# Kernel tuning notes

Hardware: AMD Instinct MI355X
Metric: run time of the kernel (lower is better)

Reference implementation:

```python
import jax, jax.numpy as jnp
import numpy as np

N, K, C = 100000, 16, 64
H, MID = 64, 16
EPS_BN = 1e-5
EPS_NORM = 1e-12

def _normalize(x, axis=-1):
    n = jnp.linalg.norm(x, axis=axis, keepdims=True)
    return x / jnp.maximum(n, EPS_NORM)

def _bn_nck(x, g, b):
    # BatchNorm1d on [N, C, K]: stats over (N, K) per channel, training mode
    m = jnp.mean(x, axis=(0, 2), keepdims=True)
    v = jnp.var(x, axis=(0, 2), keepdims=True)
    return (x - m) / jnp.sqrt(v + EPS_BN) * g[None, :, None] + b[None, :, None]

def _bn_nc(x, g, b):
    m = jnp.mean(x, axis=0, keepdims=True)
    v = jnp.var(x, axis=0, keepdims=True)
    return (x - m) / jnp.sqrt(v + EPS_BN) * g[None, :] + b[None, :]

def _conv_bn_relu(x, W, b, g, be):
    # 1x1 Conv1d: x [N, Cin, K], W [Cout, Cin]
    y = jnp.einsum('oc,nck->nok', W, x) + b[None, :, None]
    return jax.nn.relu(_bn_nck(y, g, be))

def setup_inputs():
    ks = jax.random.split(jax.random.key(0), 16)
    rn = lambda k, s: jax.random.normal(k, s, dtype=jnp.float32) * 0.05
    z = lambda n: jnp.zeros((n,), jnp.float32)
    o = lambda n: jnp.ones((n,), jnp.float32)
    return {
        'xyz': jax.random.normal(ks[0], (N, 3), jnp.float32),
        'cov': jax.random.normal(ks[1], (N, 3, 3), jnp.float32),
        'feats': jax.random.normal(ks[2], (N, C), jnp.float32),
        'knn_indices': jax.random.randint(ks[3], (N, K), 0, N),
        'fw1': rn(ks[4], (H, C)), 'fb1': z(H), 'fg1': o(H), 'fbe1': z(H),
        'fw2': rn(ks[5], (H, H)), 'fb2': z(H), 'fg2': o(H), 'fbe2': z(H),
        'ww1': rn(ks[6], (8, 14)), 'wb1': z(8), 'wg1': o(8), 'wbe1': z(8),
        'ww2': rn(ks[7], (8, 8)), 'wb2': z(8), 'wg2': o(8), 'wbe2': z(8),
        'ww3': rn(ks[8], (MID, 8)), 'wb3': z(MID), 'wg3': o(MID), 'wbe3': z(MID),
        'lin_w': rn(ks[9], (H, MID * H)), 'lin_b': z(H),
        'bng': o(H), 'bnb': z(H),
    }

def reference(xyz, cov, feats, knn_indices,
              fw1, fb1, fg1, fbe1, fw2, fb2, fg2, fbe2,
              ww1, wb1, wg1, wbe1, ww2, wb2, wg2, wbe2,
              ww3, wb3, wg3, wbe3, lin_w, lin_b, bng, bnb):
    xg = xyz[knn_indices]                      # [N,K,3] gathered positions
    loc = xg - xg[:, :1, :]                    # localized xyz (center = neighbor 0)
    cg = cov[knn_indices]                      # [N,K,3,3]
    fg = feats[knn_indices]                    # [N,K,C]

    n_alpha = fg[:, :, 3:6]                    # neighbor normals
    n_miu = n_alpha[:, 0, :]                   # center normal [N,3]
    r_hat = _normalize(loc, axis=2)
    dot_nm_rhat = jnp.einsum('nd,nkd->nk', n_miu, r_hat)
    v_miu = _normalize(n_miu[:, None, :] - dot_nm_rhat[:, :, None] * r_hat, axis=2)
    w_miu = _normalize(jnp.cross(r_hat, v_miu), axis=2)

    t1 = jnp.einsum('nkd,nd->nk', n_alpha, n_miu)
    t2 = dot_nm_rhat
    t3 = jnp.sum(r_hat * n_alpha, axis=2)
    t4 = jnp.einsum('nkd,nd->nk', loc, n_miu)
    t5 = t3
    t6 = jnp.sum(n_alpha * v_miu, axis=2)
    t7 = jnp.sum(n_alpha * w_miu, axis=2)
    t8 = jnp.sum(loc * jnp.cross(n_alpha, jnp.broadcast_to(n_miu[:, None, :], n_alpha.shape)), axis=2)
    t9 = jnp.linalg.norm(loc, axis=2)
    s1 = jnp.einsum('nkd,nkde,nke->nk', loc, cg, loc)        # per-neighbor cov quad form
    s2 = jnp.einsum('nkd,nde,nke->nk', loc, cg[:, 0], loc)   # center cov quad form

    win = jnp.concatenate([loc.transpose(0, 2, 1),
                           jnp.stack([t1, t2, t3, t4, t5, t6, t7, t8, t9, s1, s2], axis=1)],
                          axis=1)              # [N,14,K]

    w = _conv_bn_relu(win, ww1, wb1, wg1, wbe1)
    w = _conv_bn_relu(w, ww2, wb2, wg2, wbe2)
    w = _conv_bn_relu(w, ww3, wb3, wg3, wbe3)  # [N,MID,K]

    f = _conv_bn_relu(fg.transpose(0, 2, 1), fw1, fb1, fg1, fbe1)
    f = _conv_bn_relu(f, fw2, fb2, fg2, fbe2)  # [N,H,K]

    new = jnp.einsum('nhk,nmk->nhm', f, w).reshape(f.shape[0], -1)  # [N, H*MID]
    return jax.nn.relu(_bn_nc(new @ lin_w.T + lin_b, bng, bnb))
```

## Files before the change

### kernel.cpp

```cpp
#include <hip/hip_runtime.h>
#include <hip/hip_bf16.h>

typedef __hip_bfloat16 bf16;
typedef __attribute__((ext_vector_type(8))) short bf16x8;
typedef __attribute__((ext_vector_type(4))) short bf16x4;
typedef __attribute__((ext_vector_type(4))) float f32x4;

#define NPTS 100000
#define KNN 16
#define NKTOT 1600000
#define NB_W 6250
#define NB_F 1563
#define NB_P 391

#define F_Y1 28672
#define F_Z1 28688
#define F_Y2 28816
#define F_Z2 28832
#define F_Y3 28960
#define F_LIN 28992
#define CNT_BYTE 131072ull
#define ZERO_BYTES 531072ull

#define Q_Y1 0
#define Q_Y2 100000
#define Q_Y3 200000
#define Q_LIN 400000
#define Q_Z1 1200000
#define Q_Z2 1400064

#define OFS_Y1   (1ull<<20)
#define OFS_ZP1  (27ull<<20)
#define OFS_ZP2  (53ull<<20)
#define OFS_P    OFS_ZP2
#define OFS_PART (79ull<<20)
#define OFS_LWB  (86ull<<20)
#define WS_NEED  (OFS_LWB + 131072ull)

__device__ inline float bfs2f(short s) {
  unsigned int u = ((unsigned int)(unsigned short)s) << 16;
  float f; __builtin_memcpy(&f, &u, 4); return f;
}
__device__ inline short f2bfs(float x) {
  bf16 h = __float2bfloat16(x);
  short s; __builtin_memcpy(&s, &h, 2); return s;
}

__device__ inline float wred(float v) {
  #pragma unroll
  for (int o = 32; o > 0; o >>= 1) v += __shfl_xor(v, o);
  return v;
}

__global__ __launch_bounds__(256) void k0(
    const float* __restrict__ xyz, const float* __restrict__ cov,
    const float* __restrict__ feats, const float* __restrict__ linw,
    float* __restrict__ P, bf16* __restrict__ lwb) {
  const int t = threadIdx.x;
  if (blockIdx.x >= NB_P) {
    int e = (blockIdx.x - NB_P) * 1024 + t * 4;
    if (e < 65536) {
      float4 v = *(const float4*)(linw + e);
      lwb[e+0] = __float2bfloat16(v.x); lwb[e+1] = __float2bfloat16(v.y);
      lwb[e+2] = __float2bfloat16(v.z); lwb[e+3] = __float2bfloat16(v.w);
    }
    return;
  }
  int n = blockIdx.x * 256 + t;
  if (n >= NPTS) return;
  float4 o0, o1, o2, o3;
  o0.x = xyz[n*3+0]; o0.y = xyz[n*3+1]; o0.z = xyz[n*3+2]; o0.w = 0.f;
  o1.x = feats[(size_t)n*64+3]; o1.y = feats[(size_t)n*64+4]; o1.z = feats[(size_t)n*64+5];
  const float* cv = cov + (size_t)n*9;
  o1.w = cv[0];
  o2.x = cv[1]; o2.y = cv[2]; o2.z = cv[3]; o2.w = cv[4];
  o3.x = cv[5]; o3.y = cv[6]; o3.z = cv[7]; o3.w = cv[8];
  float* pr = P + (size_t)n*16;
  *(float4*)(pr+0) = o0; *(float4*)(pr+4) = o1;
  *(float4*)(pr+8) = o2; *(float4*)(pr+12) = o3;
}

__global__ __launch_bounds__(256) void k1(
    const float* __restrict__ P, const int* __restrict__ knn,
    const float* __restrict__ ww1, const float* __restrict__ wb1,
    float* __restrict__ part, int* __restrict__ cnt, bf16* __restrict__ Y1) {
  __shared__ float s_P[256][16];
  __shared__ float s_ww1t[14][8];
  __shared__ float s_ws[4][16];
  const int t = threadIdx.x;
  const long base = (long)blockIdx.x * 256;
  if (t < 112) { int c = t >> 3, h = t & 7; s_ww1t[c][h] = ww1[h * 14 + c]; }
  const int idx = knn[base + t];
  atomicAdd(&cnt[idx], 1);
  const float* pr = P + (size_t)idx * 16;
  float4 r0 = *(const float4*)(pr+0);
  float4 r1 = *(const float4*)(pr+4);
  float4 r2 = *(const float4*)(pr+8);
  float4 r3 = *(const float4*)(pr+12);
  *(float4*)&s_P[t][0] = r0; *(float4*)&s_P[t][4] = r1;
  *(float4*)&s_P[t][8] = r2; *(float4*)&s_P[t][12] = r3;
  __syncthreads();
  const int b = t & ~15;
  float lx = r0.x - s_P[b][0], ly = r0.y - s_P[b][1], lz = r0.z - s_P[b][2];
  float nmx = s_P[b][4], nmy = s_P[b][5], nmz = s_P[b][6];
  float nax = r1.x, nay = r1.y, naz = r1.z;
  float t9v = sqrtf(lx*lx + ly*ly + lz*lz);
  float rn = 1.0f / fmaxf(t9v, 1e-12f);
  float rx = lx*rn, ry = ly*rn, rz = lz*rn;
  float t2v = nmx*rx + nmy*ry + nmz*rz;
  float vx = nmx - t2v*rx, vy = nmy - t2v*ry, vz = nmz - t2v*rz;
  float vn = 1.0f / fmaxf(sqrtf(vx*vx+vy*vy+vz*vz), 1e-12f);
  vx *= vn; vy *= vn; vz *= vn;
  float wxv = ry*vz - rz*vy, wyv = rz*vx - rx*vz, wzv = rx*vy - ry*vx;
  float wn = 1.0f / fmaxf(sqrtf(wxv*wxv+wyv*wyv+wzv*wzv), 1e-12f);
  wxv *= wn; wyv *= wn; wzv *= wn;
  float t1v = nax*nmx + nay*nmy + naz*nmz;
  float t3v = rx*nax + ry*nay + rz*naz;
  float t4v = lx*nmx + ly*nmy + lz*nmz;
  float t6v = nax*vx + nay*vy + naz*vz;
  float t7v = nax*wxv + nay*wyv + naz*wzv;
  float cxx = nay*nmz - naz*nmy, cyy = naz*nmx - nax*nmz, czz = nax*nmy - nay*nmx;
  float t8v = lx*cxx + ly*cyy + lz*czz;
  float q0 = r1.w*lx + r2.x*ly + r2.y*lz;
  float q1 = r2.z*lx + r2.w*ly + r3.x*lz;
  float q2 = r3.y*lx + r3.z*ly + r3.w*lz;
  float s1v = lx*q0 + ly*q1 + lz*q2;
  float p0 = s_P[b][7]*lx  + s_P[b][8]*ly  + s_P[b][9]*lz;
  float p1 = s_P[b][10]*lx + s_P[b][11]*ly + s_P[b][12]*lz;
  float p2 = s_P[b][13]*lx + s_P[b][14]*ly + s_P[b][15]*lz;
  float s2v = lx*p0 + ly*p1 + lz*p2;
  float win[14] = {lx, ly, lz, t1v, t2v, t3v, t4v, t3v, t6v, t7v, t8v, t9v, s1v, s2v};
  float y[8];
  #pragma unroll
  for (int h = 0; h < 8; h++) y[h] = wb1[h];
  #pragma unroll
  for (int c = 0; c < 14; c++) {
    float x = win[c];
    #pragma unroll
    for (int h = 0; h < 8; h++) y[h] = fmaf(s_ww1t[c][h], x, y[h]);
  }
  const long nkg = base + t;
  bf16x8 pk;
  #pragma unroll
  for (int h = 0; h < 8; h++) pk[h] = f2bfs(y[h]);
  *(bf16x8*)&Y1[nkg * 8] = pk;
  const int w = t >> 6, lane = t & 63;
  #pragma unroll
  for (int h = 0; h < 8; h++) {
    float s = wred(y[h]);
    float q = wred(y[h] * y[h]);
    if (lane == 0) { s_ws[w][h] = s; s_ws[w][8 + h] = q; }
  }
  __syncthreads();
  if (t < 16)
    part[Q_Y1 + blockIdx.x * 16 + t] = s_ws[0][t] + s_ws[1][t] + s_ws[2][t] + s_ws[3][t];
}

__global__ __launch_bounds__(256) void kredfin(
    const float* __restrict__ part, float* __restrict__ stats,
    int qA, int nA, int cA, const float* gA, const float* beA, float mA, int fA,
    int qB, int nB, int cB, const float* gB, const float* beB, float mB, int fB) {
  int c = blockIdx.x;
  const float* p; int nblk, C, f; const float *g, *be; float M;
  if (c < cA) { p = part + qA; nblk = nA; C = cA; g = gA; be = beA; M = mA; f = fA; }
  else { c -= cA; p = part + qB; nblk = nB; C = cB; g = gB; be = beB; M = mB; f = fB; }
  const int t = threadIdx.x;
  float s = 0.f, q = 0.f;
  for (int b = t; b < nblk; b += 256) {
    s += p[(size_t)b * 2 * C + c];
    q += p[(size_t)b * 2 * C + C + c];
  }
  s = wred(s); q = wred(q);
  __shared__ float rs[4], rq[4];
  const int w = t >> 6;
  if ((t & 63) == 0) { rs[w] = s; rq[w] = q; }
  __syncthreads();
  if (t == 0) {
    s = rs[0] + rs[1] + rs[2] + rs[3];
    q = rq[0] + rq[1] + rq[2] + rq[3];
    float mean = s / M;
    float var = q / M - mean * mean;
    float scale = g[c] / sqrtf(var + 1e-5f);
    stats[f + c] = scale;
    stats[f + C + c] = be[c] - mean * scale;
  }
}

__global__ __launch_bounds__(256) void k2(
    const bf16* __restrict__ Y1, const float* __restrict__ ww2, const float* __restrict__ wb2,
    const float* __restrict__ feats, const float* __restrict__ fw1, const float* __restrict__ fb1,
    const int* __restrict__ cnt, const float* __restrict__ stats,
    float* __restrict__ part, float* __restrict__ zp1) {
  const int t = threadIdx.x;
  if (blockIdx.x < NB_W) {
    __shared__ float s_ww2t[8][8];
    __shared__ float s_sc[8], s_sh[8];
    __shared__ float s_ws[4][16];
    if (t < 64) { int c = t >> 3, h = t & 7; s_ww2t[c][h] = ww2[h*8+c]; }
    if (t < 8)  { s_sc[t] = stats[F_Y1 + t]; s_sh[t] = stats[F_Y1 + 8 + t]; }
    __syncthreads();
    const long nkg = (long)blockIdx.x * 256 + t;
    bf16x8 yv = *(const bf16x8*)&Y1[nkg * 8];
    float a[8];
    #pragma unroll
    for (int c = 0; c < 8; c++)
      a[c] = fmaxf(fmaf(s_sc[c], bfs2f(yv[c]), s_sh[c]), 0.f);
    float y2[8];
    #pragma unroll
    for (int h = 0; h < 8; h++) y2[h] = wb2[h];
    #pragma unroll
    for (int c = 0; c < 8; c++)
      #pragma unroll
      for (int h = 0; h < 8; h++) y2[h] = fmaf(s_ww2t[c][h], a[c], y2[h]);
    const int w = t >> 6, lane = t & 63;
    #pragma unroll
    for (int h = 0; h < 8; h++) {
      float s = wred(y2[h]);
      float q = wred(y2[h] * y2[h]);
      if (lane == 0) { s_ws[w][h] = s; s_ws[w][8 + h] = q; }
    }
    __syncthreads();
    if (t < 16)
      part[Q_Y2 + blockIdx.x * 16 + t] = s_ws[0][t] + s_ws[1][t] + s_ws[2][t] + s_ws[3][t];
    return;
  }
  __shared__ __align__(16) bf16 s_A[64 * 72];
  __shared__ float s_sum[64], s_sq[64];
  const int fblk = blockIdx.x - NB_W;
  const int p0 = fblk * 64;
  if (t < 64) { s_sum[t] = 0.f; s_sq[t] = 0.f; }
  for (int r = 0; r < 16; r++) {
    int e = r * 256 + t;
    int p = e >> 6, c = e & 63;
    int gp = p0 + p;
    float v = (gp < NPTS) ? feats[(size_t)gp*64 + c] : 0.f;
    s_A[p * 72 + c] = __float2bfloat16(v);
  }
  __syncthreads();
  const int wv = t >> 6, lane = t & 63, pt = lane & 15, kq = lane >> 4;
  for (int nt = 0; nt < 4; nt++) {
    f32x4 acc = {0.f, 0.f, 0.f, 0.f};
    int h = nt * 16 + pt;
    #pragma unroll
    for (int ks = 0; ks < 2; ks++) {
      bf16x8 av = *(const bf16x8*)&s_A[(wv*16 + pt) * 72 + ks*32 + kq*8];
      float4 b0 = *(const float4*)(fw1 + h*64 + ks*32 + kq*8);
      float4 b1 = *(const float4*)(fw1 + h*64 + ks*32 + kq*8 + 4);
      bf16x8 bv;
      bv[0]=f2bfs(b0.x); bv[1]=f2bfs(b0.y); bv[2]=f2bfs(b0.z); bv[3]=f2bfs(b0.w);
      bv[4]=f2bfs(b1.x); bv[5]=f2bfs(b1.y); bv[6]=f2bfs(b1.z); bv[7]=f2bfs(b1.w);
      acc = __builtin_amdgcn_mfma_f32_16x16x32_bf16(av, bv, acc, 0, 0, 0);
    }
    float bias = fb1[h];
    float ss = 0.f, qq = 0.f;
    #pragma unroll
    for (int r = 0; r < 4; r++) {
      int gp = p0 + wv*16 + kq*4 + r;
      float z = acc[r] + bias;
      if (gp < NPTS) {
        zp1[(size_t)gp*64 + h] = z;
        float w = (float)cnt[gp];
        ss += w * z; qq += w * z * z;
      }
    }
    ss += __shfl_xor(ss, 16); ss += __shfl_xor(ss, 32);
    qq += __shfl_xor(qq, 16); qq += __shfl_xor(qq, 32);
    if (lane < 16) { atomicAdd(&s_sum[h], ss); atomicAdd(&s_sq[h], qq); }
  }
  __syncthreads();
  if (t < 128)
    part[Q_Z1 + fblk * 128 + t] = (t < 64) ? s_sum[t] : s_sq[t - 64];
}

__global__ __launch_bounds__(256) void k3(
    const bf16* __restrict__ Y1,
    const float* __restrict__ ww2, const float* __restrict__ wb2,
    const float* __restrict__ ww3, const float* __restrict__ wb3,
    const float* __restrict__ zp1, const float* __restrict__ fw2, const float* __restrict__ fb2,
    const int* __restrict__ cnt, const float* __restrict__ stats,
    float* __restrict__ part, float* __restrict__ zp2) {
  const int t = threadIdx.x;
  if (blockIdx.x < NB_W) {
    __shared__ float s_ww2t[8][8];
    __shared__ float s_ww3t[8][16];
    __shared__ float s_sc1[8], s_sh1[8], s_sc2[8], s_sh2[8];
    __shared__ float s_ws[4][32];
    if (t < 64)  { int c = t >> 3, h = t & 7; s_ww2t[c][h] = ww2[h*8+c]; }
    if (t < 128) { int h = t >> 4, m = t & 15; s_ww3t[h][m] = ww3[m*8+h]; }
    if (t < 8)  { s_sc1[t] = stats[F_Y1 + t]; s_sh1[t] = stats[F_Y1 + 8 + t]; }
    if (t >= 8 && t < 16) { s_sc2[t-8] = stats[F_Y2 + (t-8)]; s_sh2[t-8] = stats[F_Y2 + 8 + (t-8)]; }
    __syncthreads();
    const long nkg = (long)blockIdx.x * 256 + t;
    bf16x8 yv = *(const bf16x8*)&Y1[nkg * 8];
    float a[8];
    #pragma unroll
    for (int c = 0; c < 8; c++)
      a[c] = fmaxf(fmaf(s_sc1[c], bfs2f(yv[c]), s_sh1[c]), 0.f);
    float y2[8];
    #pragma unroll
    for (int h = 0; h < 8; h++) y2[h] = wb2[h];
    #pragma unroll
    for (int c = 0; c < 8; c++)
      #pragma unroll
      for (int h = 0; h < 8; h++) y2[h] = fmaf(s_ww2t[c][h], a[c], y2[h]);
    float a2w[8];
    #pragma unroll
    for (int h = 0; h < 8; h++) a2w[h] = fmaxf(fmaf(s_sc2[h], y2[h], s_sh2[h]), 0.f);
    float y3[16];
    #pragma unroll
    for (int m = 0; m < 16; m++) y3[m] = wb3[m];
    #pragma unroll
    for (int h = 0; h < 8; h++)
      #pragma unroll
      for (int m = 0; m < 16; m++) y3[m] = fmaf(s_ww3t[h][m], a2w[h], y3[m]);
    const int w = t >> 6, lane = t & 63;
    #pragma unroll
    for (int m = 0; m < 16; m++) {
      float s = wred(y3[m]);
      float q = wred(y3[m] * y3[m]);
      if (lane == 0) { s_ws[w][m] = s; s_ws[w][16 + m] = q; }
    }
    __syncthreads();
    if (t < 32)
      part[Q_Y3 + blockIdx.x * 32 + t] = s_ws[0][t] + s_ws[1][t] + s_ws[2][t] + s_ws[3][t];
    return;
  }
  __shared__ __align__(16) bf16 s_A[64 * 72];
  __shared__ float s_sum[64], s_sq[64];
  __shared__ float s_sc[64], s_sh[64];
  const int fblk = blockIdx.x - NB_W;
  const int p0 = fblk * 64;
  if (t < 64) { s_sum[t] = 0.f; s_sq[t] = 0.f; s_sc[t] = stats[F_Z1 + t]; s_sh[t] = stats[F_Z1 + 64 + t]; }
  __syncthreads();
  for (int r = 0; r < 16; r++) {
    int e = r * 256 + t;
    int p = e >> 6, c = e & 63;
    int gp = p0 + p;
    float v = 0.f;
    if (gp < NPTS) v = fmaxf(fmaf(s_sc[c], zp1[(size_t)gp*64 + c], s_sh[c]), 0.f);
    s_A[p * 72 + c] = __float2bfloat16(v);
  }
  __syncthreads();
  const int wv = t >> 6, lane = t & 63, pt = lane & 15, kq = lane >> 4;
  for (int nt = 0; nt < 4; nt++) {
    f32x4 acc = {0.f, 0.f, 0.f, 0.f};
    int h = nt * 16 + pt;
    #pragma unroll
    for (int ks = 0; ks < 2; ks++) {
      bf16x8 av = *(const bf16x8*)&s_A[(wv*16 + pt) * 72 + ks*32 + kq*8];
      float4 b0 = *(const float4*)(fw2 + h*64 + ks*32 + kq*8);
      float4 b1 = *(const float4*)(fw2 + h*64 + ks*32 + kq*8 + 4);
      bf16x8 bv;
      bv[0]=f2bfs(b0.x); bv[1]=f2bfs(b0.y); bv[2]=f2bfs(b0.z); bv[3]=f2bfs(b0.w);
      bv[4]=f2bfs(b1.x); bv[5]=f2bfs(b1.y); bv[6]=f2bfs(b1.z); bv[7]=f2bfs(b1.w);
      acc = __builtin_amdgcn_mfma_f32_16x16x32_bf16(av, bv, acc, 0, 0, 0);
    }
    float bias = fb2[h];
    float ss = 0.f, qq = 0.f;
    #pragma unroll
    for (int r = 0; r < 4; r++) {
      int gp = p0 + wv*16 + kq*4 + r;
      float z = acc[r] + bias;
      if (gp < NPTS) {
        zp2[(size_t)gp*64 + h] = z;
        float w = (float)cnt[gp];
        ss += w * z; qq += w * z * z;
      }
    }
    ss += __shfl_xor(ss, 16); ss += __shfl_xor(ss, 32);
    qq += __shfl_xor(qq, 16); qq += __shfl_xor(qq, 32);
    if (lane < 16) { atomicAdd(&s_sum[h], ss); atomicAdd(&s_sq[h], qq); }
  }
  __syncthreads();
  if (t < 128)
    part[Q_Z2 + fblk * 128 + t] = (t < 64) ? s_sum[t] : s_sq[t - 64];
}

__global__ __launch_bounds__(256) void k3b(
    const float* __restrict__ zp2, const float* __restrict__ stats, bf16* __restrict__ a2) {
  long e = ((long)blockIdx.x * 256 + threadIdx.x) * 4;
  int c = (int)(e & 63);
  float4 v = *(const float4*)(zp2 + e);
  bf16x4 o;
  o[0] = f2bfs(fmaxf(fmaf(stats[F_Z2 + c+0], v.x, stats[F_Z2 + 64 + c+0]), 0.f));
  o[1] = f2bfs(fmaxf(fmaf(stats[F_Z2 + c+1], v.y, stats[F_Z2 + 64 + c+1]), 0.f));
  o[2] = f2bfs(fmaxf(fmaf(stats[F_Z2 + c+2], v.z, stats[F_Z2 + 64 + c+2]), 0.f));
  o[3] = f2bfs(fmaxf(fmaf(stats[F_Z2 + c+3], v.w, stats[F_Z2 + 64 + c+3]), 0.f));
  *(bf16x4*)&a2[e] = o;
}

__global__ __launch_bounds__(256) void k4(
    const bf16* __restrict__ Y1, const int* __restrict__ knn,
    const float* __restrict__ ww2, const float* __restrict__ wb2,
    const float* __restrict__ ww3, const float* __restrict__ wb3,
    const bf16* __restrict__ a2, const bf16* __restrict__ lwb, const float* __restrict__ linb,
    const float* __restrict__ stats, float* __restrict__ part, float* __restrict__ outp) {
  __shared__ int s_idx[256];
  __shared__ float s_ww2t[8][8];
  __shared__ float s_ww3t[8][16];
  __shared__ float s_scy1[8], s_shy1[8], s_scy2[8], s_shy2[8];
  __shared__ float s_scy3[16], s_shy3[16];
  __shared__ float s_ls[64], s_lq[64];
  __shared__ __align__(16) bf16 s_w[16 * 392];
  __shared__ __align__(16) bf16 s_new[16 * 1032];
  const int t = threadIdx.x;
  const long base = (long)blockIdx.x * 256;
  s_idx[t] = knn[base + t];
  if (t < 64)  { int c = t >> 3, h = t & 7; s_ww2t[c][h] = ww2[h*8+c]; }
  if (t < 128) { int h = t >> 4, m = t & 15; s_ww3t[h][m] = ww3[m*8+h]; }
  if (t < 8)  { s_scy1[t] = stats[F_Y1 + t]; s_shy1[t] = stats[F_Y1 + 8 + t]; }
  if (t >= 8 && t < 16) { s_scy2[t-8] = stats[F_Y2 + (t-8)]; s_shy2[t-8] = stats[F_Y2 + 8 + (t-8)]; }
  if (t >= 16 && t < 32) { s_scy3[t-16] = stats[F_Y3 + (t-16)]; s_shy3[t-16] = stats[F_Y3 + 16 + (t-16)]; }
  __syncthreads();

  {
    const long nkg = base + t;
    bf16x8 yv = *(const bf16x8*)&Y1[nkg * 8];
    float a[8];
    #pragma unroll
    for (int c = 0; c < 8; c++)
      a[c] = fmaxf(fmaf(s_scy1[c], bfs2f(yv[c]), s_shy1[c]), 0.f);
    float y2[8];
    #pragma unroll
    for (int h = 0; h < 8; h++) y2[h] = wb2[h];
    #pragma unroll
    for (int c = 0; c < 8; c++)
      #pragma unroll
      for (int h = 0; h < 8; h++) y2[h] = fmaf(s_ww2t[c][h], a[c], y2[h]);
    float a2w[8];
    #pragma unroll
    for (int h = 0; h < 8; h++) a2w[h] = fmaxf(fmaf(s_scy2[h], y2[h], s_shy2[h]), 0.f);
    float y3[16];
    #pragma unroll
    for (int m = 0; m < 16; m++) y3[m] = wb3[m];
    #pragma unroll
    for (int h = 0; h < 8; h++)
      #pragma unroll
      for (int m = 0; m < 16; m++) y3[m] = fmaf(s_ww3t[h][m], a2w[h], y3[m]);
    const int p = t >> 4, k = t & 15;
    #pragma unroll
    for (int mp = 0; mp < 8; mp++) {
      float w0 = fmaxf(fmaf(s_scy3[2*mp],   y3[2*mp],   s_shy3[2*mp]),   0.f);
      float w1 = fmaxf(fmaf(s_scy3[2*mp+1], y3[2*mp+1], s_shy3[2*mp+1]), 0.f);
      __hip_bfloat162 pk; pk.x = __float2bfloat16(w0); pk.y = __float2bfloat16(w1);
      *(__hip_bfloat162*)&s_w[p*392 + k*24 + 2*mp] = pk;
    }
  }
  __syncthreads();

  {
    const int p = t >> 4, l = t & 15;
    int idxs[16];
    #pragma unroll
    for (int k = 0; k < 16; k++) idxs[k] = s_idx[(p << 4) + k];
    bf16x4 zf[16];
    #pragma unroll
    for (int k = 0; k < 16; k++)
      zf[k] = *(const bf16x4*)(a2 + (size_t)idxs[k] * 64 + (l << 2));
    float acc[4][16];
    #pragma unroll
    for (int hj = 0; hj < 4; hj++)
      #pragma unroll
      for (int m = 0; m < 16; m++) acc[hj][m] = 0.f;
    #pragma unroll
    for (int k = 0; k < 16; k++) {
      bf16x8 w0 = *(const bf16x8*)&s_w[p*392 + k*24];
      bf16x8 w1 = *(const bf16x8*)&s_w[p*392 + k*24 + 8];
      float f0 = bfs2f(zf[k][0]);
      float f1 = bfs2f(zf[k][1]);
      float f2 = bfs2f(zf[k][2]);
      float f3 = bfs2f(zf[k][3]);
      float wf[16];
      #pragma unroll
      for (int m = 0; m < 8; m++) { wf[m] = bfs2f(w0[m]); wf[8+m] = bfs2f(w1[m]); }
      #pragma unroll
      for (int m = 0; m < 16; m++) {
        acc[0][m] = fmaf(f0, wf[m], acc[0][m]);
        acc[1][m] = fmaf(f1, wf[m], acc[1][m]);
        acc[2][m] = fmaf(f2, wf[m], acc[2][m]);
        acc[3][m] = fmaf(f3, wf[m], acc[3][m]);
      }
    }
    const int swz = (l & 7) * 8;
    #pragma unroll
    for (int hj = 0; hj < 4; hj++)
      #pragma unroll
      for (int mp = 0; mp < 8; mp++) {
        int v = hj*16 + 2*mp;
        int phys = (l << 6) + (v ^ swz);
        __hip_bfloat162 pk;
        pk.x = __float2bfloat16(acc[hj][2*mp]); pk.y = __float2bfloat16(acc[hj][2*mp+1]);
        *(__hip_bfloat162*)&s_new[p*1032 + phys] = pk;
      }
  }
  __syncthreads();

  {
    const int wv = t >> 6, lane = t & 63, pt = lane & 15, kq = lane >> 4;
    const int j = wv * 16 + pt;
    const bf16* lwrow = lwb + j * 1024;
    f32x4 acc = {0.f, 0.f, 0.f, 0.f};
    #pragma unroll 8
    for (int ks = 0; ks < 32; ks++) {
      int i = ks*32 + kq*8;
      int l2 = i >> 6, v = i & 63;
      int phys = (l2 << 6) + (v ^ ((l2 & 7) * 8));
      bf16x8 av = *(const bf16x8*)&s_new[pt*1032 + phys];
      bf16x8 bv = *(const bf16x8*)(lwrow + i);
      acc = __builtin_amdgcn_mfma_f32_16x16x32_bf16(av, bv, acc, 0, 0, 0);
    }
    float bj = linb[j];
    float ss = 0.f, qq = 0.f;
    #pragma unroll
    for (int r = 0; r < 4; r++) {
      int gp = (int)(blockIdx.x * 16) + kq*4 + r;
      float val = acc[r] + bj;
      outp[(size_t)gp*64 + j] = val;
      ss += val; qq += val * val;
    }
    ss += __shfl_xor(ss, 16); ss += __shfl_xor(ss, 32);
    qq += __shfl_xor(qq, 16); qq += __shfl_xor(qq, 32);
    if (lane < 16) { s_ls[j] = ss; s_lq[j] = qq; }
  }
  __syncthreads();
  if (t < 128)
    part[Q_LIN + blockIdx.x * 128 + t] = (t < 64) ? s_ls[t] : s_lq[t - 64];
}

__global__ __launch_bounds__(256) void k6(float* __restrict__ outp, const float* __restrict__ stats) {
  long e = (long)blockIdx.x * 256 + threadIdx.x;
  int j = (int)(e & 63);
  float sc = stats[F_LIN + j], sh = stats[F_LIN + 64 + j];
  float v = outp[e];
  outp[e] = fmaxf(fmaf(sc, v, sh), 0.f);
}

__global__ void k_wsfail(float* outp, float mb) {
  outp[threadIdx.x] = -mb;
}

extern "C" void kernel_launch(void* const* d_in, const int* in_sizes, int n_in,
                              void* d_out, int out_size, void* d_ws, size_t ws_size,
                              hipStream_t stream) {
  const float* xyz  = (const float*)d_in[0];
  const float* cov  = (const float*)d_in[1];
  const float* feats= (const float*)d_in[2];
  const int*   knn  = (const int*)d_in[3];
  const float* fw1  = (const float*)d_in[4];
  const float* fb1  = (const float*)d_in[5];
  const float* fg1  = (const float*)d_in[6];
  const float* fbe1 = (const float*)d_in[7];
  const float* fw2  = (const float*)d_in[8];
  const float* fb2  = (const float*)d_in[9];
  const float* fg2  = (const float*)d_in[10];
  const float* fbe2 = (const float*)d_in[11];
  const float* ww1  = (const float*)d_in[12];
  const float* wb1  = (const float*)d_in[13];
  const float* wg1  = (const float*)d_in[14];
  const float* wbe1 = (const float*)d_in[15];
  const float* ww2  = (const float*)d_in[16];
  const float* wb2  = (const float*)d_in[17];
  const float* wg2  = (const float*)d_in[18];
  const float* wbe2 = (const float*)d_in[19];
  const float* ww3  = (const float*)d_in[20];
  const float* wb3  = (const float*)d_in[21];
  const float* wg3  = (const float*)d_in[22];
  const float* wbe3 = (const float*)d_in[23];
  const float* linw = (const float*)d_in[24];
  const float* linb = (const float*)d_in[25];
  const float* bng  = (const float*)d_in[26];
  const float* bnb  = (const float*)d_in[27];

  float* outp = (float*)d_out;
  if (ws_size < WS_NEED) {
    hipLaunchKernelGGL(k_wsfail, dim3(1), dim3(256), 0, stream, outp, (float)(ws_size >> 20));
    return;
  }
  char* ws = (char*)d_ws;
  float* stats = (float*)ws;
  int*   cnt   = (int*)(ws + CNT_BYTE);
  bf16*  Y1    = (bf16*)(ws + OFS_Y1);
  float* zp1   = (float*)(ws + OFS_ZP1);
  bf16*  a2    = (bf16*)(ws + OFS_ZP1);
  float* zp2   = (float*)(ws + OFS_ZP2);
  float* P     = (float*)(ws + OFS_P);
  float* part  = (float*)(ws + OFS_PART);
  bf16*  lwb   = (bf16*)(ws + OFS_LWB);

  hipMemsetAsync(d_ws, 0, ZERO_BYTES, stream);
  hipLaunchKernelGGL(k0, dim3(NB_P + 64), dim3(256), 0, stream,
                     xyz, cov, feats, linw, P, lwb);
  hipLaunchKernelGGL(k1, dim3(NB_W), dim3(256), 0, stream,
                     P, knn, ww1, wb1, part, cnt, Y1);
  hipLaunchKernelGGL(kredfin, dim3(16), dim3(256), 0, stream, part, stats,
                     Q_Y1, NB_W, 8, wg1, wbe1, (float)NKTOT, F_Y1,
                     Q_Y1, NB_W, 8, wg1, wbe1, (float)NKTOT, F_Y1);
  hipLaunchKernelGGL(k2, dim3(NB_W + NB_F), dim3(256), 0, stream,
                     Y1, ww2, wb2, feats, fw1, fb1, cnt, stats, part, zp1);
  hipLaunchKernelGGL(kredfin, dim3(72), dim3(256), 0, stream, part, stats,
                     Q_Y2, NB_W, 8, wg2, wbe2, (float)NKTOT, F_Y2,
                     Q_Z1, NB_F, 64, fg1, fbe1, (float)NKTOT, F_Z1);
  hipLaunchKernelGGL(k3, dim3(NB_W + NB_F), dim3(256), 0, stream,
                     Y1, ww2, wb2, ww3, wb3, zp1, fw2, fb2, cnt, stats, part, zp2);
  hipLaunchKernelGGL(kredfin, dim3(80), dim3(256), 0, stream, part, stats,
                     Q_Y3, NB_W, 16, wg3, wbe3, (float)NKTOT, F_Y3,
                     Q_Z2, NB_F, 64, fg2, fbe2, (float)NKTOT, F_Z2);
  hipLaunchKernelGGL(k3b, dim3(6250), dim3(256), 0, stream, zp2, stats, a2);
  hipLaunchKernelGGL(k4, dim3(NB_W), dim3(256), 0, stream,
                     Y1, knn, ww2, wb2, ww3, wb3, a2, lwb, linb, stats, part, outp);
  hipLaunchKernelGGL(kredfin, dim3(128), dim3(256), 0, stream, part, stats,
                     Q_LIN, NB_W, 64, bng, bnb, (float)NPTS, F_LIN,
                     Q_LIN, NB_W, 64, bng, bnb, (float)NPTS, F_LIN);
  hipLaunchKernelGGL(k6, dim3(25000), dim3(256), 0, stream, outp, stats);
}
```

Baseline: 682.7 us.

## Gather neighbor rows directly into LDS via global_load_lds in k1 and k4

Replaces register-staged gathers with direct global-to-LDS async loads (global_load_lds, 16 bytes per lane) in both k1 (point records) and k4 (a2 feature rows). In k4, the gathered feature rows are staged in the s_new buffer, which is later reused for the MFMA operand, so an extra barrier is added before it is overwritten. The aim is to cut VGPR pressure and let the gather latency overlap with the other prologue work. In k1 the P record layout in LDS is split into four planes. The costs are an extra __syncthreads in k4 and a reliance on the wave-uniform LDS base semantics of the builtin being correct.

```diff
diff --git a/kernel.cpp b/kernel.cpp
--- a/kernel.cpp
+++ b/kernel.cpp
@@ -44,6 +44,12 @@
 __device__ inline short f2bfs(float x) {
   bf16 h = __float2bfloat16(x);
   short s; __builtin_memcpy(&s, &h, 2); return s;
+}
+
+__device__ inline void gl_lds16(const void* g, void* l) {
+  __builtin_amdgcn_global_load_lds(
+      (const __attribute__((address_space(1))) void*)g,
+      (__attribute__((address_space(3))) void*)l, 16, 0, 0);
 }
 
 __device__ inline float wred(float v) {
@@ -84,25 +90,26 @@
     const float* __restrict__ P, const int* __restrict__ knn,
     const float* __restrict__ ww1, const float* __restrict__ wb1,
     float* __restrict__ part, int* __restrict__ cnt, bf16* __restrict__ Y1) {
-  __shared__ float s_P[256][16];
+  __shared__ float s_Pn[4][256][4];
   __shared__ float s_ww1t[14][8];
   __shared__ float s_ws[4][16];
   const int t = threadIdx.x;
+  const int w = t >> 6;
   const long base = (long)blockIdx.x * 256;
+  const int idx = knn[base + t];
+  #pragma unroll
+  for (int c = 0; c < 4; c++)
+    gl_lds16(P + (size_t)idx * 16 + c * 4, &s_Pn[c][w * 64][0]);
+  atomicAdd(&cnt[idx], 1);
   if (t < 112) { int c = t >> 3, h = t & 7; s_ww1t[c][h] = ww1[h * 14 + c]; }
-  const int idx = knn[base + t];
-  atomicAdd(&cnt[idx], 1);
-  const float* pr = P + (size_t)idx * 16;
-  float4 r0 = *(const float4*)(pr+0);
-  float4 r1 = *(const float4*)(pr+4);
-  float4 r2 = *(const float4*)(pr+8);
-  float4 r3 = *(const float4*)(pr+12);
-  *(float4*)&s_P[t][0] = r0; *(float4*)&s_P[t][4] = r1;
-  *(float4*)&s_P[t][8] = r2; *(float4*)&s_P[t][12] = r3;
   __syncthreads();
   const int b = t & ~15;
-  float lx = r0.x - s_P[b][0], ly = r0.y - s_P[b][1], lz = r0.z - s_P[b][2];
-  float nmx = s_P[b][4], nmy = s_P[b][5], nmz = s_P[b][6];
+  float4 r0 = *(const float4*)&s_Pn[0][t][0];
+  float4 r1 = *(const float4*)&s_Pn[1][t][0];
+  float4 r2 = *(const float4*)&s_Pn[2][t][0];
+  float4 r3 = *(const float4*)&s_Pn[3][t][0];
+  float lx = r0.x - s_Pn[0][b][0], ly = r0.y - s_Pn[0][b][1], lz = r0.z - s_Pn[0][b][2];
+  float nmx = s_Pn[1][b][0], nmy = s_Pn[1][b][1], nmz = s_Pn[1][b][2];
   float nax = r1.x, nay = r1.y, naz = r1.z;
   float t9v = sqrtf(lx*lx + ly*ly + lz*lz);
   float rn = 1.0f / fmaxf(t9v, 1e-12f);
@@ -125,9 +132,9 @@
   float q1 = r2.z*lx + r2.w*ly + r3.x*lz;
   float q2 = r3.y*lx + r3.z*ly + r3.w*lz;
   float s1v = lx*q0 + ly*q1 + lz*q2;
-  float p0 = s_P[b][7]*lx  + s_P[b][8]*ly  + s_P[b][9]*lz;
-  float p1 = s_P[b][10]*lx + s_P[b][11]*ly + s_P[b][12]*lz;
-  float p2 = s_P[b][13]*lx + s_P[b][14]*ly + s_P[b][15]*lz;
+  float p0 = s_Pn[1][b][3]*lx + s_Pn[2][b][0]*ly + s_Pn[2][b][1]*lz;
+  float p1 = s_Pn[2][b][2]*lx + s_Pn[2][b][3]*ly + s_Pn[3][b][0]*lz;
+  float p2 = s_Pn[3][b][1]*lx + s_Pn[3][b][2]*ly + s_Pn[3][b][3]*lz;
   float s2v = lx*p0 + ly*p1 + lz*p2;
   float win[14] = {lx, ly, lz, t1v, t2v, t3v, t4v, t3v, t6v, t7v, t8v, t9v, s1v, s2v};
   float y[8];
@@ -144,7 +151,7 @@
   #pragma unroll
   for (int h = 0; h < 8; h++) pk[h] = f2bfs(y[h]);
   *(bf16x8*)&Y1[nkg * 8] = pk;
-  const int w = t >> 6, lane = t & 63;
+  const int lane = t & 63;
   #pragma unroll
   for (int h = 0; h < 8; h++) {
     float s = wred(y[h]);
@@ -395,7 +402,6 @@
     const float* __restrict__ ww3, const float* __restrict__ wb3,
     const bf16* __restrict__ a2, const bf16* __restrict__ lwb, const float* __restrict__ linb,
     const float* __restrict__ stats, float* __restrict__ part, float* __restrict__ outp) {
-  __shared__ int s_idx[256];
   __shared__ float s_ww2t[8][8];
   __shared__ float s_ww3t[8][16];
   __shared__ float s_scy1[8], s_shy1[8], s_scy2[8], s_shy2[8];
@@ -404,8 +410,15 @@
   __shared__ __align__(16) bf16 s_w[16 * 392];
   __shared__ __align__(16) bf16 s_new[16 * 1032];
   const int t = threadIdx.x;
+  const int w = t >> 6, lane = t & 63;
   const long base = (long)blockIdx.x * 256;
-  s_idx[t] = knn[base + t];
+  const int myidx = knn[base + t];
+  #pragma unroll
+  for (int c = 0; c < 8; c++) {
+    int src = c * 8 + (lane >> 3);
+    int ridx = __shfl(myidx, src);
+    gl_lds16(a2 + (size_t)ridx * 64 + (lane & 7) * 8, &s_new[(w * 64 + c * 8) * 64]);
+  }
   if (t < 64)  { int c = t >> 3, h = t & 7; s_ww2t[c][h] = ww2[h*8+c]; }
   if (t < 128) { int h = t >> 4, m = t & 15; s_ww3t[h][m] = ww3[m*8+h]; }
   if (t < 8)  { s_scy1[t] = stats[F_Y1 + t]; s_shy1[t] = stats[F_Y1 + 8 + t]; }
@@ -448,28 +461,22 @@
   }
   __syncthreads();
 
+  float acc[4][16];
   {
     const int p = t >> 4, l = t & 15;
-    int idxs[16];
-    #pragma unroll
-    for (int k = 0; k < 16; k++) idxs[k] = s_idx[(p << 4) + k];
-    bf16x4 zf[16];
-    #pragma unroll
-    for (int k = 0; k < 16; k++)
-      zf[k] = *(const bf16x4*)(a2 + (size_t)idxs[k] * 64 + (l << 2));
-    float acc[4][16];
     #pragma unroll
     for (int hj = 0; hj < 4; hj++)
       #pragma unroll
       for (int m = 0; m < 16; m++) acc[hj][m] = 0.f;
     #pragma unroll
     for (int k = 0; k < 16; k++) {
+      bf16x4 zf = *(const bf16x4*)&s_new[(p * 16 + k) * 64 + l * 4];
       bf16x8 w0 = *(const bf16x8*)&s_w[p*392 + k*24];
       bf16x8 w1 = *(const bf16x8*)&s_w[p*392 + k*24 + 8];
-      float f0 = bfs2f(zf[k][0]);
-      float f1 = bfs2f(zf[k][1]);
-      float f2 = bfs2f(zf[k][2]);
-      float f3 = bfs2f(zf[k][3]);
+      float f0 = bfs2f(zf[0]);
+      float f1 = bfs2f(zf[1]);
+      float f2 = bfs2f(zf[2]);
+      float f3 = bfs2f(zf[3]);
       float wf[16];
       #pragma unroll
       for (int m = 0; m < 8; m++) { wf[m] = bfs2f(w0[m]); wf[8+m] = bfs2f(w1[m]); }
@@ -481,6 +488,11 @@
         acc[3][m] = fmaf(f3, wf[m], acc[3][m]);
       }
     }
+  }
+  __syncthreads();
+
+  {
+    const int p = t >> 4, l = t & 15;
     const int swz = (l & 7) * 8;
     #pragma unroll
     for (int hj = 0; hj < 4; hj++)
@@ -496,10 +508,10 @@
   __syncthreads();
 
   {
-    const int wv = t >> 6, lane = t & 63, pt = lane & 15, kq = lane >> 4;
+    const int wv = t >> 6, pt = lane & 15, kq = lane >> 4;
     const int j = wv * 16 + pt;
     const bf16* lwrow = lwb + j * 1024;
-    f32x4 acc = {0.f, 0.f, 0.f, 0.f};
+    f32x4 macc = {0.f, 0.f, 0.f, 0.f};
     #pragma unroll 8
     for (int ks = 0; ks < 32; ks++) {
       int i = ks*32 + kq*8;
@@ -507,14 +519,14 @@
       int phys = (l2 << 6) + (v ^ ((l2 & 7) * 8));
       bf16x8 av = *(const bf16x8*)&s_new[pt*1032 + phys];
       bf16x8 bv = *(const bf16x8*)(lwrow + i);
-      acc = __builtin_amdgcn_mfma_f32_16x16x32_bf16(av, bv, acc, 0, 0, 0);
+      macc = __builtin_amdgcn_mfma_f32_16x16x32_bf16(av, bv, macc, 0, 0, 0);
     }
     float bj = linb[j];
     float ss = 0.f, qq = 0.f;
     #pragma unroll
     for (int r = 0; r < 4; r++) {
       int gp = (int)(blockIdx.x * 16) + kq*4 + r;
-      float val = acc[r] + bj;
+      float val = macc[r] + bj;
       outp[(size_t)gp*64 + j] = val;
       ss += val; qq += val * val;
     }
```

New measurement: 676.9 us. Within noise of the previous version (-0.8%).
